# Optimization experiments

Hardware: AMD Instinct MI355X
Metric: run time of the kernel (lower is better)

## Reference

```python
import jax, jax.numpy as jnp
import numpy as np

K = 7          # neighborhood kernel size (7x7)
NH = 8         # num heads


def _nbr_idx(n):
    # NATTEN-style clamped windows: window start = clip(i - K//2, 0, n-K)
    pos = jnp.arange(n)
    start = jnp.clip(pos - K // 2, 0, n - K)          # (n,)
    idx = start[:, None] + jnp.arange(K)[None, :]     # (n, K) absolute key positions
    rel = idx - pos[:, None] + (K - 1)                # (n, K) in [0, 2K-2] for rpb lookup
    return idx, rel


def _forward(x, w_qkv, b_qkv, rpb, w_proj, b_proj, w_fc1, b_fc1, w_fc2, b_fc2):
    B, C, H, W = x.shape
    hd = C // NH
    scale = hd ** -0.5

    # ---- neighborhood attention (norm0 = Identity) ----
    xp = jnp.transpose(x, (0, 2, 3, 1))                           # (B,H,W,C)
    qkv = xp @ w_qkv + b_qkv                                      # (B,H,W,3C)
    qkv = qkv.reshape(B, H, W, 3, NH, hd)
    q = qkv[:, :, :, 0] * scale                                   # (B,H,W,nh,hd)
    k = qkv[:, :, :, 1]
    v = qkv[:, :, :, 2]

    idx_h, rel_h = _nbr_idx(H)                                    # (H,K)
    idx_w, rel_w = _nbr_idx(W)                                    # (W,K)

    # gather 7x7 neighborhoods: (B,H,K,W,K,nh,hd)
    k_nbr = k[:, idx_h][:, :, :, idx_w]
    v_nbr = v[:, idx_h][:, :, :, idx_w]

    # attention logits: (B,H,W,nh,K,K)
    attn = jnp.einsum('bxynd,bxiyjnd->bxynij', q, k_nbr)
    # relative positional bias: rpb (nh, 2K-1, 2K-1) -> (nh,H,K,W,K)
    bias = rpb[:, rel_h][:, :, :, rel_w]                          # (nh,H,K,W,K)
    attn = attn + jnp.transpose(bias, (1, 3, 0, 2, 4))[None]      # (B,H,W,nh,K,K)

    attn = jax.nn.softmax(attn.reshape(B, H, W, NH, K * K), axis=-1)
    attn = attn.reshape(B, H, W, NH, K, K)

    out = jnp.einsum('bxynij,bxiyjnd->bxynd', attn, v_nbr)        # (B,H,W,nh,hd)
    out = out.reshape(B, H, W, C) @ w_proj + b_proj               # (B,H,W,C)
    x1 = jnp.transpose(out, (0, 3, 1, 2)) + x                     # residual skip0

    # ---- MLP (1x1-conv style, channels-first; norm1 = Identity) ----
    h = jnp.einsum('bchw,cf->bfhw', x1, w_fc1) + b_fc1[None, :, None, None]
    h = jax.nn.gelu(h, approximate=False)                         # torch nn.GELU (erf)
    y = jnp.einsum('bfhw,fc->bchw', h, w_fc2) + b_fc2[None, :, None, None]
    return y + x1                                                 # residual skip1


def setup_inputs() -> dict:
    key = jax.random.key(0)
    B, C, H, W = 1, 256, 64, 128
    hid = int(C * 2.0)
    ks = jax.random.split(key, 8)
    s = 0.02
    return {
        'x': jax.random.normal(ks[0], (B, C, H, W), jnp.float32),
        'w_qkv': jax.random.normal(ks[1], (C, 3 * C), jnp.float32) * s,
        'b_qkv': jnp.zeros((3 * C,), jnp.float32),
        'rpb': jax.random.normal(ks[2], (NH, 2 * K - 1, 2 * K - 1), jnp.float32) * s,
        'w_proj': jax.random.normal(ks[3], (C, C), jnp.float32) * s,
        'b_proj': jnp.zeros((C,), jnp.float32),
        'w_fc1': jax.random.normal(ks[4], (C, hid), jnp.float32) * s,
        'b_fc1': jnp.zeros((hid,), jnp.float32),
        'w_fc2': jax.random.normal(ks[5], (hid, C), jnp.float32) * s,
        'b_fc2': jnp.zeros((C,), jnp.float32),
    }


def reference(x, w_qkv, b_qkv, rpb, w_proj, b_proj, w_fc1, b_fc1, w_fc2, b_fc2):
    return _forward(x, w_qkv, b_qkv, rpb, w_proj, b_proj, w_fc1, b_fc1, w_fc2, b_fc2)
```

## Files before the change

kernel.cpp:

```cpp
#include <hip/hip_runtime.h>

typedef unsigned short ushort;
typedef short bf16x8 __attribute__((ext_vector_type(8)));
typedef float f32x4 __attribute__((ext_vector_type(4)));

static __device__ __forceinline__ ushort f2b(float f) {
  unsigned u = __builtin_bit_cast(unsigned, f);
  u = (u + 0x7fffu + ((u >> 16) & 1u)) >> 16;
  return (ushort)u;
}
static __device__ __forceinline__ float b2f(ushort b) {
  return __builtin_bit_cast(float, (unsigned)b << 16);
}

static __device__ __forceinline__ void gll16(const ushort* g, ushort* l) {
  __builtin_amdgcn_global_load_lds(
      (const __attribute__((address_space(1))) void*)g,
      (__attribute__((address_space(3))) void*)l, 16, 0, 0);
}

__global__ __launch_bounds__(256) void prep_kernel(
    const float* __restrict__ x,
    const float* __restrict__ w_qkv, const float* __restrict__ w_proj,
    const float* __restrict__ w_fc1, const float* __restrict__ w_fc2,
    ushort* __restrict__ xb, ushort* __restrict__ wqkvT,
    ushort* __restrict__ wprojT, ushort* __restrict__ wfc1T,
    ushort* __restrict__ wfc2T)
{
  __shared__ float tile[32][33];
  int t = blockIdx.x;
  const float* src; ushort* dst; int R, Nc, r0, c0;
  if (t < 2048)              { src = x;      dst = xb;     R = 256; Nc = 8192; r0 = (t >> 8) * 32; c0 = (t & 255) * 32; }
  else if ((t -= 2048) < 192){ src = w_qkv;  dst = wqkvT;  R = 256; Nc = 768;  r0 = (t / 24) * 32; c0 = (t % 24) * 32; }
  else if ((t -= 192) < 64)  { src = w_proj; dst = wprojT; R = 256; Nc = 256;  r0 = (t / 8) * 32;  c0 = (t % 8) * 32; }
  else if ((t -= 64) < 128)  { src = w_fc1;  dst = wfc1T;  R = 256; Nc = 512;  r0 = (t / 16) * 32; c0 = (t % 16) * 32; }
  else           { t -= 128;   src = w_fc2;  dst = wfc2T;  R = 512; Nc = 256;  r0 = (t / 8) * 32;  c0 = (t % 8) * 32; }

  const int tx = threadIdx.x & 31, ty = threadIdx.x >> 5;
  #pragma unroll
  for (int i = 0; i < 4; i++)
    tile[ty + i * 8][tx] = src[(size_t)(r0 + ty + i * 8) * Nc + c0 + tx];
  __syncthreads();
  #pragma unroll
  for (int i = 0; i < 4; i++)
    dst[(size_t)(c0 + ty + i * 8) * R + r0 + tx] = f2b(tile[tx][ty + i * 8]);
}

template<int EPI, int KD>
__global__ __launch_bounds__(256) void gemm_mfma(
    const ushort* __restrict__ A, const ushort* __restrict__ Bt,
    const float* __restrict__ bias, const float* __restrict__ R,
    const ushort* __restrict__ RS,
    void* __restrict__ C0, void* __restrict__ C1,
    int M, int N)
{
  __shared__ __attribute__((aligned(16))) ushort As[64 * 128];
  __shared__ __attribute__((aligned(16))) ushort Bs[64 * 128];

  const int bm = blockIdx.y * 64;
  const int bn = blockIdx.x * 64;
  const int t  = threadIdx.x;
  const int w    = t >> 6;
  const int lane = t & 63;
  const int wm = (w & 1) * 32;
  const int wn = (w >> 1) * 32;
  const int lm = lane & 15;
  const int kq = lane >> 4;

  const int rl  = lane >> 4;
  const int cbx = (lane & 15) << 4;
  const int xr  = (lm & 7) << 4;

  f32x4 acc[2][2] = {};

  #pragma unroll
  for (int k0 = 0; k0 < KD; k0 += 128) {
    #pragma unroll
    for (int s = 0; s < 4; s++) {
      const int c = w * 4 + s;
      const int r = c * 4 + rl;
      const int off = (cbx ^ ((r & 7) << 4)) >> 1;
      gll16(A  + (size_t)(bm + r) * KD + k0 + off, As + c * 512);
      gll16(Bt + (size_t)(bn + r) * KD + k0 + off, Bs + c * 512);
    }
    __syncthreads();

    #pragma unroll
    for (int ks = 0; ks < 4; ks++) {
      const int kb = ks * 64 + (kq << 4);
      const int cs = kb ^ xr;
      bf16x8 a0 = *(const bf16x8*)((const char*)As + (wm + lm)      * 256 + cs);
      bf16x8 a1 = *(const bf16x8*)((const char*)As + (wm + 16 + lm) * 256 + cs);
      bf16x8 b0 = *(const bf16x8*)((const char*)Bs + (wn + lm)      * 256 + cs);
      bf16x8 b1 = *(const bf16x8*)((const char*)Bs + (wn + 16 + lm) * 256 + cs);
      acc[0][0] = __builtin_amdgcn_mfma_f32_16x16x32_bf16(a0, b0, acc[0][0], 0, 0, 0);
      acc[0][1] = __builtin_amdgcn_mfma_f32_16x16x32_bf16(a0, b1, acc[0][1], 0, 0, 0);
      acc[1][0] = __builtin_amdgcn_mfma_f32_16x16x32_bf16(a1, b0, acc[1][0], 0, 0, 0);
      acc[1][1] = __builtin_amdgcn_mfma_f32_16x16x32_bf16(a1, b1, acc[1][1], 0, 0, 0);
    }
    __syncthreads();
  }

  #pragma unroll
  for (int ti = 0; ti < 2; ti++) {
    #pragma unroll
    for (int tj = 0; tj < 2; tj++) {
      const int n  = bn + wn + tj * 16 + lm;
      const int m0 = bm + wm + ti * 16 + kq * 4;
      if (EPI == 0) {
        if (n < 512) {
          #pragma unroll
          for (int r = 0; r < 4; r++)
            ((ushort*)C0)[(size_t)(m0 + r) * N + n] = f2b(acc[ti][tj][r] + bias[n]);
        } else {
          ushort4 st;
          st.x = f2b(acc[ti][tj][0] + bias[n]);
          st.y = f2b(acc[ti][tj][1] + bias[n]);
          st.z = f2b(acc[ti][tj][2] + bias[n]);
          st.w = f2b(acc[ti][tj][3] + bias[n]);
          *(ushort4*)((ushort*)C1 + (size_t)(n - 512) * 8192 + m0) = st;
        }
      }
    }
  }
}

__global__ __launch_bounds__(256, 4) void natt_mfma(
    const ushort* __restrict__ qkv, const ushort* __restrict__ vT,
    const float* __restrict__ rpb, ushort* __restrict__ att)
{
  __shared__ __attribute__((aligned(16))) ushort Plds[4][7][16][40];
  __shared__ float Rlds[4][176];

  const int w    = threadIdx.x >> 6;
  const int lane = threadIdx.x & 63;
  const int l  = lane & 15;
  const int q  = lane >> 4;
  const int tile = blockIdx.x;
  const int n    = blockIdx.y * 4 + w;
  const int ph  = tile >> 3;
  const int pw0 = (tile & 7) << 4;
  const int p0  = ph * 128 + pw0;

  int sh = ph - 3;  sh = sh < 0 ? 0 : (sh > 57 ? 57 : sh);
  int sb = pw0 - 3; sb = sb < 0 ? 0 : sb;
  const int sba = sb & ~7;

  const float L2E = 1.44269504f;
  for (int idx = lane; idx < 169; idx += 64)
    Rlds[w][idx] = rpb[n * 169 + idx] * L2E;

  bf16x8 qf = *(const bf16x8*)(qkv + (size_t)(p0 + l) * 768 + n * 32 + q * 8);

  const float KSC = 0.17677669529663689f * 1.44269504f;
  const int relh0 = sh - ph + 6;
  float rsum[4] = {0.f, 0.f, 0.f, 0.f};

  #pragma unroll
  for (int h = 0; h < 2; h++) {
    f32x4 s[7] = {};
    #pragma unroll
    for (int i = 0; i < 7; i++) {
      const int rowp = (sh + i) * 128;
      int jc = sba + h * 16 + l;
      jc = jc > 127 ? 127 : jc;
      bf16x8 kf = *(const bf16x8*)(qkv + (size_t)(rowp + jc) * 768 + 256 + n * 32 + q * 8);
      s[i] = __builtin_amdgcn_mfma_f32_16x16x32_bf16(qf, kf, s[i], 0, 0, 0);
    }
    #pragma unroll
    for (int r = 0; r < 4; r++) {
      const int pw = pw0 + q * 4 + r;
      int sw = pw - 3; sw = sw < 0 ? 0 : (sw > 121 ? 121 : sw);
      const int jc = sba + h * 16 + l;
      const bool valid = (unsigned)(jc - sw) <= 6u;
      int relw = jc - pw + 6;
      relw = relw < 0 ? 0 : (relw > 12 ? 12 : relw);
      #pragma unroll
      for (int i = 0; i < 7; i++) {
        float b = Rlds[w][(relh0 + i) * 13 + relw];
        float v = s[i][r] * KSC + b;
        v = valid ? v : -1e30f;
        float e = exp2f(v);
        rsum[r] += e;
        Plds[w][i][q * 4 + r][h * 16 + l] = f2b(e);
      }
    }
  }

  #pragma unroll
  for (int r = 0; r < 4; r++) {
    rsum[r] += __shfl_xor(rsum[r], 1);
    rsum[r] += __shfl_xor(rsum[r], 2);
    rsum[r] += __shfl_xor(rsum[r], 4);
    rsum[r] += __shfl_xor(rsum[r], 8);
  }

  f32x4 o[2] = {};
  #pragma unroll
  for (int i = 0; i < 7; i++) {
    bf16x8 pf = *(const bf16x8*)(&Plds[w][i][l][q * 8]);
    const int rowp = (sh + i) * 128;
    #pragma unroll
    for (int dh = 0; dh < 2; dh++) {
      bf16x8 vf = *(const bf16x8*)(vT + (size_t)(n * 32 + dh * 16 + l) * 8192
                                      + rowp + sba + q * 8);
      o[dh] = __builtin_amdgcn_mfma_f32_16x16x32_bf16(pf, vf, o[dh], 0, 0, 0);
    }
  }

  #pragma unroll
  for (int r = 0; r < 4; r++) {
    const float inv = 1.0f / rsum[r];
    #pragma unroll
    for (int dh = 0; dh < 2; dh++)
      att[(size_t)(p0 + q * 4 + r) * 256 + n * 32 + dh * 16 + l] = f2b(o[dh][r] * inv);
  }
}

__global__ __launch_bounds__(512) void mlp_fused(
    const ushort* __restrict__ att, const ushort* __restrict__ wprojT,
    const ushort* __restrict__ wfc1T, const ushort* __restrict__ wfc2T,
    const float* __restrict__ b_proj, const float* __restrict__ b_fc1,
    const float* __restrict__ b_fc2, const float* __restrict__ xres,
    float* __restrict__ out)
{
  __shared__ __attribute__((aligned(16))) ushort As[32 * 128];
  __shared__ __attribute__((aligned(16))) ushort Bs[256 * 128];
  __shared__ __attribute__((aligned(16))) ushort X1[32 * 256];
  __shared__ __attribute__((aligned(16))) ushort Hs[32 * 256];

  const int bm   = blockIdx.x * 32;
  const int t    = threadIdx.x;
  const int w    = t >> 6;
  const int lane = t & 63;
  const int lm   = lane & 15;
  const int kq   = lane >> 4;
  const int wm   = (w & 1) * 16;
  const int wn   = (w >> 1) * 64;

  const int rl  = lane >> 4;
  const int swl = (lane & 15) << 3;

  f32x4 acc_o[4] = {};

  {
    f32x4 acc_p[4] = {};
    #pragma unroll
    for (int kt = 0; kt < 2; kt++) {
      {
        const int m = w * 4 + rl;
        gll16(att + (size_t)(bm + m) * 256 + kt * 128 + (swl ^ ((m & 7) << 3)),
              As + w * 512);
      }
      #pragma unroll
      for (int s = 0; s < 8; s++) {
        const int c = w * 8 + s;
        const int n = c * 4 + rl;
        gll16(wprojT + (size_t)n * 256 + kt * 128 + (swl ^ ((n & 7) << 3)),
              Bs + c * 512);
      }
      __syncthreads();
      #pragma unroll
      for (int ks = 0; ks < 4; ks++) {
        const int kc = ks * 32 + kq * 8;
        const int ar = wm + lm;
        bf16x8 a = *(const bf16x8*)(&As[ar * 128 + (kc ^ ((ar & 7) << 3))]);
        #pragma unroll
        for (int tj = 0; tj < 4; tj++) {
          const int n = wn + tj * 16 + lm;
          bf16x8 b = *(const bf16x8*)(&Bs[n * 128 + (kc ^ ((n & 7) << 3))]);
          acc_p[tj] = __builtin_amdgcn_mfma_f32_16x16x32_bf16(a, b, acc_p[tj], 0, 0, 0);
        }
      }
      __syncthreads();
    }
    #pragma unroll
    for (int tj = 0; tj < 4; tj++) {
      const int n = wn + tj * 16 + lm;
      #pragma unroll
      for (int r = 0; r < 4; r++) {
        const int m = wm + kq * 4 + r;
        float v = acc_p[tj][r] + b_proj[n] + xres[(size_t)n * 8192 + bm + m];
        X1[m * 256 + n] = f2b(v);
      }
    }
    __syncthreads();
  }

  #pragma unroll
  for (int hf = 0; hf < 2; hf++) {
    f32x4 acc_h[4] = {};
    #pragma unroll
    for (int kt = 0; kt < 2; kt++) {
      #pragma unroll
      for (int s = 0; s < 8; s++) {
        const int c = w * 8 + s;
        const int n = c * 4 + rl;
        gll16(wfc1T + (size_t)(hf * 256 + n) * 256 + kt * 128 + (swl ^ ((n & 7) << 3)),
              Bs + c * 512);
      }
      __syncthreads();
      #pragma unroll
      for (int ks = 0; ks < 4; ks++) {
        const int kc = ks * 32 + kq * 8;
        const int ar = wm + lm;
        bf16x8 a = *(const bf16x8*)(&X1[ar * 256 + kt * 128 + kc]);
        #pragma unroll
        for (int tj = 0; tj < 4; tj++) {
          const int n = wn + tj * 16 + lm;
          bf16x8 b = *(const bf16x8*)(&Bs[n * 128 + (kc ^ ((n & 7) << 3))]);
          acc_h[tj] = __builtin_amdgcn_mfma_f32_16x16x32_bf16(a, b, acc_h[tj], 0, 0, 0);
        }
      }
      __syncthreads();
    }
    #pragma unroll
    for (int tj = 0; tj < 4; tj++) {
      const int n = wn + tj * 16 + lm;
      #pragma unroll
      for (int r = 0; r < 4; r++) {
        const int m = wm + kq * 4 + r;
        float v = acc_h[tj][r] + b_fc1[hf * 256 + n];
        v = 0.5f * v * (1.0f + erff(v * 0.70710678118f));
        Hs[m * 256 + n] = f2b(v);
      }
    }
    __syncthreads();

    #pragma unroll
    for (int kt = 0; kt < 2; kt++) {
      #pragma unroll
      for (int s = 0; s < 8; s++) {
        const int c = w * 8 + s;
        const int n = c * 4 + rl;
        gll16(wfc2T + (size_t)n * 512 + hf * 256 + kt * 128 + (swl ^ ((n & 7) << 3)),
              Bs + c * 512);
      }
      __syncthreads();
      #pragma unroll
      for (int ks = 0; ks < 4; ks++) {
        const int kc = ks * 32 + kq * 8;
        const int ar = wm + lm;
        bf16x8 a = *(const bf16x8*)(&Hs[ar * 256 + kt * 128 + kc]);
        #pragma unroll
        for (int tj = 0; tj < 4; tj++) {
          const int n = wn + tj * 16 + lm;
          bf16x8 b = *(const bf16x8*)(&Bs[n * 128 + (kc ^ ((n & 7) << 3))]);
          acc_o[tj] = __builtin_amdgcn_mfma_f32_16x16x32_bf16(a, b, acc_o[tj], 0, 0, 0);
        }
      }
      __syncthreads();
    }
  }

  #pragma unroll
  for (int tj = 0; tj < 4; tj++) {
    const int n  = wn + tj * 16 + lm;
    const int m0 = wm + kq * 4;
    float4 v;
    float* vp = &v.x;
    #pragma unroll
    for (int r = 0; r < 4; r++)
      vp[r] = acc_o[tj][r] + b_fc2[n] + b2f(X1[(m0 + r) * 256 + n]);
    *(float4*)(out + (size_t)n * 8192 + bm + m0) = v;
  }
}

extern "C" void kernel_launch(void* const* d_in, const int* in_sizes, int n_in,
                              void* d_out, int out_size, void* d_ws, size_t ws_size,
                              hipStream_t stream)
{
  const float* x      = (const float*)d_in[0];
  const float* w_qkv  = (const float*)d_in[1];
  const float* b_qkv  = (const float*)d_in[2];
  const float* rpb    = (const float*)d_in[3];
  const float* w_proj = (const float*)d_in[4];
  const float* b_proj = (const float*)d_in[5];
  const float* w_fc1  = (const float*)d_in[6];
  const float* b_fc1  = (const float*)d_in[7];
  const float* w_fc2  = (const float*)d_in[8];
  const float* b_fc2  = (const float*)d_in[9];
  float* out = (float*)d_out;

  const int M = 8192;
  char* ws = (char*)d_ws;
  ushort* xb     = (ushort*)(ws);
  ushort* qkv    = (ushort*)(ws + 4194304);
  ushort* wqkvT  = (ushort*)(ws + 20971520);
  ushort* wprojT = (ushort*)(ws + 21364736);
  ushort* wfc1T  = (ushort*)(ws + 21495808);
  ushort* wfc2T  = (ushort*)(ws + 21757952);
  ushort* vT     = (ushort*)(ws + 22020096);
  ushort* att = xb;

  dim3 blk(256);

  prep_kernel<<<dim3(2560), blk, 0, stream>>>(
      x, w_qkv, w_proj, w_fc1, w_fc2, xb, wqkvT, wprojT, wfc1T, wfc2T);

  gemm_mfma<0, 256><<<dim3(768 / 64, M / 64), blk, 0, stream>>>(
      xb, wqkvT, b_qkv, nullptr, nullptr, qkv, vT, M, 768);

  natt_mfma<<<dim3(512, 2), blk, 0, stream>>>(qkv, vT, rpb, att);

  mlp_fused<<<dim3(256), dim3(512), 0, stream>>>(
      att, wprojT, wfc1T, wfc2T, b_proj, b_fc1, b_fc2, x, out);
}
```

Measured before the change: 132.7 us.

## Halve MLP weight staging tile to cut LDS, swizzle X1/Hs, read attention directly

The fused proj+MLP kernel now stages 128-row weight tiles instead of 256-row ones and splits each GEMM's N dimension into two halves. This cuts shared memory from roughly 96KB to 64KB per block, which may allow more resident blocks. X1 and Hs are written and read with an XOR swizzle to reduce LDS bank conflicts. The attention A-operand is loaded straight from global memory and the residual is read as float4. The cost is twice as many barriers and staging rounds per block, and the uncached global A loads are repeated for each N half.

```diff
diff --git a/kernel.cpp b/kernel.cpp
--- a/kernel.cpp
+++ b/kernel.cpp
@@ -224,8 +224,7 @@
     const float* __restrict__ b_fc2, const float* __restrict__ xres,
     float* __restrict__ out)
 {
-  __shared__ __attribute__((aligned(16))) ushort As[32 * 128];
-  __shared__ __attribute__((aligned(16))) ushort Bs[256 * 128];
+  __shared__ __attribute__((aligned(16))) ushort Bs[128 * 128];
   __shared__ __attribute__((aligned(16))) ushort X1[32 * 256];
   __shared__ __attribute__((aligned(16))) ushort Hs[32 * 256];
 
@@ -236,133 +235,139 @@
   const int lm   = lane & 15;
   const int kq   = lane >> 4;
   const int wm   = (w & 1) * 16;
-  const int wn   = (w >> 1) * 64;
+  const int wnn  = (w >> 1) * 32;
 
   const int rl  = lane >> 4;
   const int swl = (lane & 15) << 3;
 
+  auto stageB = [&](const ushort* __restrict__ src, int ldk, int row0, int col0) {
+    #pragma unroll
+    for (int s = 0; s < 4; s++) {
+      const int c = w * 4 + s;
+      const int n = c * 4 + rl;
+      gll16(src + (size_t)(row0 + n) * ldk + col0 + (swl ^ ((n & 7) << 3)),
+            Bs + c * 512);
+    }
+  };
+
   f32x4 acc_o[4] = {};
 
-  {
-    f32x4 acc_p[4] = {};
+  #pragma unroll
+  for (int nh = 0; nh < 2; nh++) {
+    f32x4 accp[2] = {};
     #pragma unroll
     for (int kt = 0; kt < 2; kt++) {
-      {
-        const int m = w * 4 + rl;
-        gll16(att + (size_t)(bm + m) * 256 + kt * 128 + (swl ^ ((m & 7) << 3)),
-              As + w * 512);
-      }
-      #pragma unroll
-      for (int s = 0; s < 8; s++) {
-        const int c = w * 8 + s;
-        const int n = c * 4 + rl;
-        gll16(wprojT + (size_t)n * 256 + kt * 128 + (swl ^ ((n & 7) << 3)),
-              Bs + c * 512);
-      }
+      stageB(wprojT, 256, nh * 128, kt * 128);
       __syncthreads();
       #pragma unroll
       for (int ks = 0; ks < 4; ks++) {
         const int kc = ks * 32 + kq * 8;
-        const int ar = wm + lm;
-        bf16x8 a = *(const bf16x8*)(&As[ar * 128 + (kc ^ ((ar & 7) << 3))]);
+        bf16x8 a = *(const bf16x8*)(att + (size_t)(bm + wm + lm) * 256 + kt * 128 + kc);
         #pragma unroll
-        for (int tj = 0; tj < 4; tj++) {
-          const int n = wn + tj * 16 + lm;
+        for (int tj = 0; tj < 2; tj++) {
+          const int n = wnn + tj * 16 + lm;
           bf16x8 b = *(const bf16x8*)(&Bs[n * 128 + (kc ^ ((n & 7) << 3))]);
-          acc_p[tj] = __builtin_amdgcn_mfma_f32_16x16x32_bf16(a, b, acc_p[tj], 0, 0, 0);
+          accp[tj] = __builtin_amdgcn_mfma_f32_16x16x32_bf16(a, b, accp[tj], 0, 0, 0);
         }
       }
       __syncthreads();
     }
     #pragma unroll
-    for (int tj = 0; tj < 4; tj++) {
-      const int n = wn + tj * 16 + lm;
+    for (int tj = 0; tj < 2; tj++) {
+      const int n  = nh * 128 + wnn + tj * 16 + lm;
+      const int m0 = wm + kq * 4;
+      const float bp = b_proj[n];
+      float4 xr = *(const float4*)(xres + (size_t)n * 8192 + bm + m0);
+      const float* xp = &xr.x;
       #pragma unroll
       for (int r = 0; r < 4; r++) {
-        const int m = wm + kq * 4 + r;
-        float v = acc_p[tj][r] + b_proj[n] + xres[(size_t)n * 8192 + bm + m];
-        X1[m * 256 + n] = f2b(v);
+        const int m = m0 + r;
+        X1[m * 256 + (n ^ ((m & 7) << 3))] = f2b(accp[tj][r] + bp + xp[r]);
+      }
+    }
+  }
+  __syncthreads();
+
+  #pragma unroll
+  for (int hf = 0; hf < 2; hf++) {
+    #pragma unroll
+    for (int nh = 0; nh < 2; nh++) {
+      f32x4 acch[2] = {};
+      #pragma unroll
+      for (int kt = 0; kt < 2; kt++) {
+        stageB(wfc1T, 256, hf * 256 + nh * 128, kt * 128);
+        __syncthreads();
+        #pragma unroll
+        for (int ks = 0; ks < 4; ks++) {
+          const int kc = ks * 32 + kq * 8;
+          const int ar = wm + lm;
+          const int ac = kt * 128 + kc;
+          bf16x8 a = *(const bf16x8*)(&X1[ar * 256 + (ac ^ ((ar & 7) << 3))]);
+          #pragma unroll
+          for (int tj = 0; tj < 2; tj++) {
+            const int n = wnn + tj * 16 + lm;
+            bf16x8 b = *(const bf16x8*)(&Bs[n * 128 + (kc ^ ((n & 7) << 3))]);
+            acch[tj] = __builtin_amdgcn_mfma_f32_16x16x32_bf16(a, b, acch[tj], 0, 0, 0);
+          }
+        }
+        __syncthreads();
+      }
+      #pragma unroll
+      for (int tj = 0; tj < 2; tj++) {
+        const int n  = nh * 128 + wnn + tj * 16 + lm;
+        const float bf = b_fc1[hf * 256 + n];
+        #pragma unroll
+        for (int r = 0; r < 4; r++) {
+          const int m = wm + kq * 4 + r;
+          float v = acch[tj][r] + bf;
+          v = 0.5f * v * (1.0f + erff(v * 0.70710678118f));
+          Hs[m * 256 + (n ^ ((m & 7) << 3))] = f2b(v);
+        }
       }
     }
     __syncthreads();
-  }
-
-  #pragma unroll
-  for (int hf = 0; hf < 2; hf++) {
-    f32x4 acc_h[4] = {};
-    #pragma unroll
-    for (int kt = 0; kt < 2; kt++) {
-      #pragma unroll
-      for (int s = 0; s < 8; s++) {
-        const int c = w * 8 + s;
-        const int n = c * 4 + rl;
-        gll16(wfc1T + (size_t)(hf * 256 + n) * 256 + kt * 128 + (swl ^ ((n & 7) << 3)),
-              Bs + c * 512);
-      }
-      __syncthreads();
-      #pragma unroll
-      for (int ks = 0; ks < 4; ks++) {
-        const int kc = ks * 32 + kq * 8;
-        const int ar = wm + lm;
-        bf16x8 a = *(const bf16x8*)(&X1[ar * 256 + kt * 128 + kc]);
+
+    #pragma unroll
+    for (int nh = 0; nh < 2; nh++) {
+      #pragma unroll
+      for (int kt = 0; kt < 2; kt++) {
+        stageB(wfc2T, 512, nh * 128, hf * 256 + kt * 128);
+        __syncthreads();
         #pragma unroll
-        for (int tj = 0; tj < 4; tj++) {
-          const int n = wn + tj * 16 + lm;
-          bf16x8 b = *(const bf16x8*)(&Bs[n * 128 + (kc ^ ((n & 7) << 3))]);
-          acc_h[tj] = __builtin_amdgcn_mfma_f32_16x16x32_bf16(a, b, acc_h[tj], 0, 0, 0);
+        for (int ks = 0; ks < 4; ks++) {
+          const int kc = ks * 32 + kq * 8;
+          const int ar = wm + lm;
+          const int ac = kt * 128 + kc;
+          bf16x8 a = *(const bf16x8*)(&Hs[ar * 256 + (ac ^ ((ar & 7) << 3))]);
+          #pragma unroll
+          for (int tj = 0; tj < 2; tj++) {
+            const int n = wnn + tj * 16 + lm;
+            bf16x8 b = *(const bf16x8*)(&Bs[n * 128 + (kc ^ ((n & 7) << 3))]);
+            acc_o[nh * 2 + tj] =
+                __builtin_amdgcn_mfma_f32_16x16x32_bf16(a, b, acc_o[nh * 2 + tj], 0, 0, 0);
+          }
         }
-      }
-      __syncthreads();
-    }
-    #pragma unroll
-    for (int tj = 0; tj < 4; tj++) {
-      const int n = wn + tj * 16 + lm;
+        __syncthreads();
+      }
+    }
+  }
+
+  #pragma unroll
+  for (int nh = 0; nh < 2; nh++) {
+    #pragma unroll
+    for (int tj = 0; tj < 2; tj++) {
+      const int n  = nh * 128 + wnn + tj * 16 + lm;
+      const int m0 = wm + kq * 4;
+      const float bf = b_fc2[n];
+      float4 v;
+      float* vp = &v.x;
       #pragma unroll
       for (int r = 0; r < 4; r++) {
-        const int m = wm + kq * 4 + r;
-        float v = acc_h[tj][r] + b_fc1[hf * 256 + n];
-        v = 0.5f * v * (1.0f + erff(v * 0.70710678118f));
-        Hs[m * 256 + n] = f2b(v);
-      }
-    }
-    __syncthreads();
-
-    #pragma unroll
-    for (int kt = 0; kt < 2; kt++) {
-      #pragma unroll
-      for (int s = 0; s < 8; s++) {
-        const int c = w * 8 + s;
-        const int n = c * 4 + rl;
-        gll16(wfc2T + (size_t)n * 512 + hf * 256 + kt * 128 + (swl ^ ((n & 7) << 3)),
-              Bs + c * 512);
-      }
-      __syncthreads();
-      #pragma unroll
-      for (int ks = 0; ks < 4; ks++) {
-        const int kc = ks * 32 + kq * 8;
-        const int ar = wm + lm;
-        bf16x8 a = *(const bf16x8*)(&Hs[ar * 256 + kt * 128 + kc]);
-        #pragma unroll
-        for (int tj = 0; tj < 4; tj++) {
-          const int n = wn + tj * 16 + lm;
-          bf16x8 b = *(const bf16x8*)(&Bs[n * 128 + (kc ^ ((n & 7) << 3))]);
-          acc_o[tj] = __builtin_amdgcn_mfma_f32_16x16x32_bf16(a, b, acc_o[tj], 0, 0, 0);
-        }
-      }
-      __syncthreads();
-    }
-  }
-
-  #pragma unroll
-  for (int tj = 0; tj < 4; tj++) {
-    const int n  = wn + tj * 16 + lm;
-    const int m0 = wm + kq * 4;
-    float4 v;
-    float* vp = &v.x;
-    #pragma unroll
-    for (int r = 0; r < 4; r++)
-      vp[r] = acc_o[tj][r] + b_fc2[n] + b2f(X1[(m0 + r) * 256 + n]);
-    *(float4*)(out + (size_t)n * 8192 + bm + m0) = v;
+        const int m = m0 + r;
+        vp[r] = acc_o[nh * 2 + tj][r] + bf + b2f(X1[m * 256 + (n ^ ((m & 7) << 3))]);
+      }
+      *(float4*)(out + (size_t)n * 8192 + bm + m0) = v;
+    }
   }
 }
 
```

Measured after the change: 138.6 us. +4.4%, slower.
